# Kernel tuning notes

Measured on AMD Instinct MI355X. Metric: run time of the kernel, lower is better.

The kernel has to match this reference:

```python
import jax, jax.numpy as jnp
import numpy as np

N_NODES = 100000
N_EDGES = 1000000
NODE_DIM = 64
HIDDEN_DIM = 128


def setup_inputs() -> dict:
    key = jax.random.key(0)
    ks = jax.random.split(key, 9)
    x = jax.random.normal(ks[0], (N_NODES, NODE_DIM), dtype=jnp.float32)
    y = jax.random.normal(ks[1], (N_NODES, NODE_DIM), dtype=jnp.float32)
    edge_index = jax.random.randint(ks[2], (2, N_EDGES), 0, N_NODES, dtype=jnp.int64)
    pos_x = jax.random.normal(ks[3], (N_NODES, 3), dtype=jnp.float32)
    pos_y = jax.random.normal(ks[4], (N_NODES, 3), dtype=jnp.float32)
    in_dim = NODE_DIM * 2 + 1
    # Kaiming-uniform-ish init like torch Linear
    lim1 = 1.0 / np.sqrt(in_dim)
    lim2 = 1.0 / np.sqrt(HIDDEN_DIM)
    W1 = jax.random.uniform(ks[5], (in_dim, HIDDEN_DIM), jnp.float32, -lim1, lim1)
    b1 = jax.random.uniform(ks[6], (HIDDEN_DIM,), jnp.float32, -lim1, lim1)
    W2 = jax.random.uniform(ks[7], (HIDDEN_DIM, 1), jnp.float32, -lim2, lim2)
    b2 = jax.random.uniform(ks[8], (1,), jnp.float32, -lim2, lim2)
    return {"x": x, "y": y, "edge_index": edge_index, "pos_x": pos_x,
            "pos_y": pos_y, "W1": W1, "b1": b1, "W2": W2, "b2": b2}


def reference(x, y, edge_index, pos_x, pos_y, W1, b1, W2, b2):
    src = edge_index[0]
    dst = edge_index[1]
    # per-edge euclidean distance between endpoint positions  [E]
    d = pos_x[src] - pos_y[dst]                      # [E, 3]
    dist = jnp.sqrt(jnp.sum(d * d, axis=1))          # [E]
    # gather + concat: [E, node_dim*2 + 1]
    mlp_in = jnp.concatenate([x[src], y[dst], dist[:, None]], axis=1)
    h = jax.nn.relu(mlp_in @ W1 + b1)                # [E, hidden]
    out = jax.nn.relu(h @ W2 + b2)                   # [E, 1]
    return out
```

## Files before the change

### kernel.cpp

```cpp
#include <hip/hip_runtime.h>
#include <hip/hip_bf16.h>


constexpr int NDIM  = 64;
constexpr int HID   = 128;
constexpr int KPAD  = 136;

typedef __attribute__((ext_vector_type(8))) short  short8;
typedef __attribute__((ext_vector_type(4))) int    int4v;
typedef __attribute__((ext_vector_type(4))) float  floatx4;

__device__ __forceinline__ short f2bf(float f) {
    union { __hip_bfloat16 h; short s; } cv;
    cv.h = __float2bfloat16(f);
    return cv.s;
}

__device__ __forceinline__ int pack2(float a, float b) {
    union { __hip_bfloat162 h; int u; } cv;
    cv.h = __float22bfloat162_rn(float2{a, b});
    return cv.u;
}

__global__ __launch_bounds__(256) void edge_mlp_kernel(
    const float* __restrict__ x, const float* __restrict__ y,
    const int*  __restrict__ ei, const float* __restrict__ px,
    const float* __restrict__ py, const float* __restrict__ W1,
    const float* __restrict__ b1, const float* __restrict__ W2,
    const float* __restrict__ b2, float* __restrict__ out, int E)
{
    __shared__ __align__(16) short Wt[HID * KPAD];

    const int tid = threadIdx.x;

    for (int base = 0; base < HID * HID; base += 256 * 8) {
        float f[8];
#pragma unroll
        for (int u = 0; u < 8; ++u) f[u] = W1[base + u * 256 + tid];
#pragma unroll
        for (int u = 0; u < 8; ++u) {
            int i = base + u * 256 + tid;
            Wt[(i & 127) * KPAD + (i >> 7)] = f2bf(f[u]);
        }
    }
    __syncthreads();

    const int lane = tid & 63;
    const int wave = tid >> 6;
    const int quad = lane >> 4;
    const int lm   = lane & 15;

    short8 bfrag[8][4];
#pragma unroll
    for (int t = 0; t < 8; ++t) {
        const int n = t * 16 + lm;
#pragma unroll
        for (int s = 0; s < 4; ++s) {
            const int k0 = s * 32 + quad * 8;
            bfrag[t][s] = *reinterpret_cast<const short8*>(&Wt[n * KPAD + k0]);
        }
    }

    float b1v[8], w2v[8], w1rv[8];
#pragma unroll
    for (int t = 0; t < 8; ++t) {
        const int n = t * 16 + lm;
        b1v[t]  = b1[n];
        w2v[t]  = W2[n];
        w1rv[t] = W1[128 * HID + n];
    }
    const float b2s = b2[0];

    const int* __restrict__ srcp = ei;
    const int* __restrict__ dstp = ei + E;

    const int ntile_cnt = E / 64;
    for (int tile = blockIdx.x; tile < ntile_cnt; tile += gridDim.x) {
        const int m_base = tile * 64 + wave * 16;
        int m = m_base + lm;
        if (m >= E) m = E - 1;
        const int src = srcp[m];
        const int dst = dstp[m];

        const float dx = px[src * 3 + 0] - py[dst * 3 + 0];
        const float dy = px[src * 3 + 1] - py[dst * 3 + 1];
        const float dz = px[src * 3 + 2] - py[dst * 3 + 2];
        const float dist = sqrtf(dx * dx + dy * dy + dz * dz);

        short8 afrag[4];
#pragma unroll
        for (int s = 0; s < 4; ++s) {
            const int kk = s * 32 + quad * 8;
            const float* rp = (s < 2) ? (x + src * NDIM + kk)
                                      : (y + dst * NDIM + (kk - 64));
            const floatx4 f0 = *reinterpret_cast<const floatx4*>(rp);
            const floatx4 f1 = *reinterpret_cast<const floatx4*>(rp + 4);
            union { int4v i; short8 s8; } cv;
            cv.i.x = pack2(f0.x, f0.y);
            cv.i.y = pack2(f0.z, f0.w);
            cv.i.z = pack2(f1.x, f1.y);
            cv.i.w = pack2(f1.z, f1.w);
            afrag[s] = cv.s8;
        }

        floatx4 acc[8];
#pragma unroll
        for (int t = 0; t < 8; ++t) acc[t] = floatx4{0.f, 0.f, 0.f, 0.f};
#pragma unroll
        for (int s = 0; s < 4; ++s) {
#pragma unroll
            for (int t = 0; t < 8; ++t) {
                acc[t] = __builtin_amdgcn_mfma_f32_16x16x32_bf16(
                    afrag[s], bfrag[t][s], acc[t], 0, 0, 0);
            }
        }

        const float dm0 = __shfl(dist, quad * 4 + 0, 64);
        const float dm1 = __shfl(dist, quad * 4 + 1, 64);
        const float dm2 = __shfl(dist, quad * 4 + 2, 64);
        const float dm3 = __shfl(dist, quad * 4 + 3, 64);

        float p0 = 0.f, p1 = 0.f, p2 = 0.f, p3 = 0.f;
#pragma unroll
        for (int t = 0; t < 8; ++t) {
            float h;
            h = acc[t][0] + dm0 * w1rv[t] + b1v[t]; h = fmaxf(h, 0.f); p0 += h * w2v[t];
            h = acc[t][1] + dm1 * w1rv[t] + b1v[t]; h = fmaxf(h, 0.f); p1 += h * w2v[t];
            h = acc[t][2] + dm2 * w1rv[t] + b1v[t]; h = fmaxf(h, 0.f); p2 += h * w2v[t];
            h = acc[t][3] + dm3 * w1rv[t] + b1v[t]; h = fmaxf(h, 0.f); p3 += h * w2v[t];
        }
#pragma unroll
        for (int off = 1; off < 16; off <<= 1) {
            p0 += __shfl_xor(p0, off, 64);
            p1 += __shfl_xor(p1, off, 64);
            p2 += __shfl_xor(p2, off, 64);
            p3 += __shfl_xor(p3, off, 64);
        }
        if (lm < 4) {
            const float v = (lm == 0) ? p0 : (lm == 1) ? p1 : (lm == 2) ? p2 : p3;
            const int e = m_base + quad * 4 + lm;
            if (e < E) out[e] = fmaxf(v + b2s, 0.f);
        }
    }
}

extern "C" void kernel_launch(void* const* d_in, const int* in_sizes, int n_in,
                              void* d_out, int out_size, void* d_ws, size_t ws_size,
                              hipStream_t stream)
{
    const float* x  = (const float*)d_in[0];
    const float* y  = (const float*)d_in[1];
    const int*   ei = (const int*)  d_in[2];
    const float* px = (const float*)d_in[3];
    const float* py = (const float*)d_in[4];
    const float* W1 = (const float*)d_in[5];
    const float* b1 = (const float*)d_in[6];
    const float* W2 = (const float*)d_in[7];
    const float* b2 = (const float*)d_in[8];
    float* out = (float*)d_out;
    const int E = in_sizes[2] / 2;

    edge_mlp_kernel<<<dim3(1024), dim3(256), 0, stream>>>(
        x, y, ei, px, py, W1, b1, W2, b2, out, E);
}
```

Measured before the change: 193.3 us.

## Stream W1 fragments from LDS, fold dist and bias into MFMA, two edge groups per wave

Stops holding all 32 W1 B-fragments in registers. Each B fragment is now read from LDS inside the loop and reused across two 16-edge groups per wave, with tiles growing from 64 to 128 edges. The distance column and bias b1 are folded into a fifth K-slice MFMA (dist, 1.0 padded with zeros), so the per-element FMA epilogue goes away, and the launch moves to 768 blocks with launch_bounds(256,3). The aim is lower register pressure for higher occupancy and more memory-level parallelism on the gathers. In exchange it adds LDS read traffic, an extra MFMA per tile, and bf16 rounding of dist and b1.

```diff
diff --git a/kernel.cpp b/kernel.cpp
--- a/kernel.cpp
+++ b/kernel.cpp
@@ -22,7 +22,18 @@
     return cv.u;
 }
 
-__global__ __launch_bounds__(256) void edge_mlp_kernel(
+__device__ __forceinline__ short8 make_afrag(const float* rp) {
+    const floatx4 f0 = *reinterpret_cast<const floatx4*>(rp);
+    const floatx4 f1 = *reinterpret_cast<const floatx4*>(rp + 4);
+    union { int4v i; short8 s8; } cv;
+    cv.i.x = pack2(f0.x, f0.y);
+    cv.i.y = pack2(f0.z, f0.w);
+    cv.i.z = pack2(f1.x, f1.y);
+    cv.i.w = pack2(f1.z, f1.w);
+    return cv.s8;
+}
+
+__global__ __launch_bounds__(256, 3) void edge_mlp_kernel(
     const float* __restrict__ x, const float* __restrict__ y,
     const int*  __restrict__ ei, const float* __restrict__ px,
     const float* __restrict__ py, const float* __restrict__ W1,
@@ -43,6 +54,13 @@
             Wt[(i & 127) * KPAD + (i >> 7)] = f2bf(f[u]);
         }
     }
+    if (tid < HID) {
+        const int n = tid;
+        Wt[n * KPAD + 128] = f2bf(W1[128 * HID + n]);
+        Wt[n * KPAD + 129] = f2bf(b1[n]);
+#pragma unroll
+        for (int j = 130; j < 136; ++j) Wt[n * KPAD + j] = 0;
+    }
     __syncthreads();
 
     const int lane = tid & 63;
@@ -50,84 +68,94 @@
     const int quad = lane >> 4;
     const int lm   = lane & 15;
 
-    short8 bfrag[8][4];
-#pragma unroll
-    for (int t = 0; t < 8; ++t) {
-        const int n = t * 16 + lm;
-#pragma unroll
-        for (int s = 0; s < 4; ++s) {
-            const int k0 = s * 32 + quad * 8;
-            bfrag[t][s] = *reinterpret_cast<const short8*>(&Wt[n * KPAD + k0]);
-        }
-    }
-
-    float b1v[8], w2v[8], w1rv[8];
-#pragma unroll
-    for (int t = 0; t < 8; ++t) {
-        const int n = t * 16 + lm;
-        b1v[t]  = b1[n];
-        w2v[t]  = W2[n];
-        w1rv[t] = W1[128 * HID + n];
-    }
+    float w2v[8];
+#pragma unroll
+    for (int t = 0; t < 8; ++t) w2v[t] = W2[t * 16 + lm];
     const float b2s = b2[0];
 
     const int* __restrict__ srcp = ei;
     const int* __restrict__ dstp = ei + E;
 
-    const int ntile_cnt = E / 64;
-    for (int tile = blockIdx.x; tile < ntile_cnt; tile += gridDim.x) {
-        const int m_base = tile * 64 + wave * 16;
-        int m = m_base + lm;
-        if (m >= E) m = E - 1;
-        const int src = srcp[m];
-        const int dst = dstp[m];
-
-        const float dx = px[src * 3 + 0] - py[dst * 3 + 0];
-        const float dy = px[src * 3 + 1] - py[dst * 3 + 1];
-        const float dz = px[src * 3 + 2] - py[dst * 3 + 2];
-        const float dist = sqrtf(dx * dx + dy * dy + dz * dz);
-
-        short8 afrag[4];
+    const int sel5 = (quad == 0) ? 128 : 0;
+
+    const int ntiles = (E + 127) / 128;
+    for (int tile = blockIdx.x; tile < ntiles; tile += gridDim.x) {
+        const int mb = tile * 128 + wave * 32;
+        int m0 = mb + lm;       if (m0 >= E) m0 = E - 1;
+        int m1 = mb + 16 + lm;  if (m1 >= E) m1 = E - 1;
+        const int src0 = srcp[m0], dst0 = dstp[m0];
+        const int src1 = srcp[m1], dst1 = dstp[m1];
+
+        const float dx0 = px[src0 * 3 + 0] - py[dst0 * 3 + 0];
+        const float dy0 = px[src0 * 3 + 1] - py[dst0 * 3 + 1];
+        const float dz0 = px[src0 * 3 + 2] - py[dst0 * 3 + 2];
+        const float dist0 = sqrtf(dx0 * dx0 + dy0 * dy0 + dz0 * dz0);
+        const float dx1 = px[src1 * 3 + 0] - py[dst1 * 3 + 0];
+        const float dy1 = px[src1 * 3 + 1] - py[dst1 * 3 + 1];
+        const float dz1 = px[src1 * 3 + 2] - py[dst1 * 3 + 2];
+        const float dist1 = sqrtf(dx1 * dx1 + dy1 * dy1 + dz1 * dz1);
+
+        short8 fa[4], fb[4];
 #pragma unroll
         for (int s = 0; s < 4; ++s) {
             const int kk = s * 32 + quad * 8;
-            const float* rp = (s < 2) ? (x + src * NDIM + kk)
-                                      : (y + dst * NDIM + (kk - 64));
-            const floatx4 f0 = *reinterpret_cast<const floatx4*>(rp);
-            const floatx4 f1 = *reinterpret_cast<const floatx4*>(rp + 4);
-            union { int4v i; short8 s8; } cv;
-            cv.i.x = pack2(f0.x, f0.y);
-            cv.i.y = pack2(f0.z, f0.w);
-            cv.i.z = pack2(f1.x, f1.y);
-            cv.i.w = pack2(f1.z, f1.w);
-            afrag[s] = cv.s8;
-        }
-
-        floatx4 acc[8];
-#pragma unroll
-        for (int t = 0; t < 8; ++t) acc[t] = floatx4{0.f, 0.f, 0.f, 0.f};
-#pragma unroll
-        for (int s = 0; s < 4; ++s) {
-#pragma unroll
-            for (int t = 0; t < 8; ++t) {
-                acc[t] = __builtin_amdgcn_mfma_f32_16x16x32_bf16(
-                    afrag[s], bfrag[t][s], acc[t], 0, 0, 0);
-            }
-        }
-
-        const float dm0 = __shfl(dist, quad * 4 + 0, 64);
-        const float dm1 = __shfl(dist, quad * 4 + 1, 64);
-        const float dm2 = __shfl(dist, quad * 4 + 2, 64);
-        const float dm3 = __shfl(dist, quad * 4 + 3, 64);
+            fa[s] = make_afrag((s < 2) ? (x + src0 * NDIM + kk) : (y + dst0 * NDIM + (kk - 64)));
+            fb[s] = make_afrag((s < 2) ? (x + src1 * NDIM + kk) : (y + dst1 * NDIM + (kk - 64)));
+        }
+        short8 fa4, fb4;
+        {
+            union { int4v i; short8 s8; } ca, cb;
+            const int d0 = (quad == 0) ? pack2(dist0, 1.0f) : 0;
+            const int d1 = (quad == 0) ? pack2(dist1, 1.0f) : 0;
+            ca.i = int4v{d0, 0, 0, 0};
+            cb.i = int4v{d1, 0, 0, 0};
+            fa4 = ca.s8; fb4 = cb.s8;
+        }
+
+        floatx4 accA[8], accB[8];
+#pragma unroll
+        for (int t = 0; t < 8; ++t) {
+            accA[t] = floatx4{0.f, 0.f, 0.f, 0.f};
+            accB[t] = floatx4{0.f, 0.f, 0.f, 0.f};
+        }
+
+        int zoff = 0;
+        asm volatile("" : "+v"(zoff));
+        const short* wr  = Wt + zoff + lm * KPAD + quad * 8;
+        const short* wr5 = Wt + zoff + lm * KPAD + sel5;
+
+#pragma unroll
+        for (int t = 0; t < 8; ++t) {
+            const short* base = wr + t * (16 * KPAD);
+            const short8 bg0 = *reinterpret_cast<const short8*>(base);
+            const short8 bg1 = *reinterpret_cast<const short8*>(base + 32);
+            const short8 bg2 = *reinterpret_cast<const short8*>(base + 64);
+            const short8 bg3 = *reinterpret_cast<const short8*>(base + 96);
+            const short8 bg4 = *reinterpret_cast<const short8*>(wr5 + t * (16 * KPAD));
+            accA[t] = __builtin_amdgcn_mfma_f32_16x16x32_bf16(fa[0], bg0, accA[t], 0, 0, 0);
+            accB[t] = __builtin_amdgcn_mfma_f32_16x16x32_bf16(fb[0], bg0, accB[t], 0, 0, 0);
+            accA[t] = __builtin_amdgcn_mfma_f32_16x16x32_bf16(fa[1], bg1, accA[t], 0, 0, 0);
+            accB[t] = __builtin_amdgcn_mfma_f32_16x16x32_bf16(fb[1], bg1, accB[t], 0, 0, 0);
+            accA[t] = __builtin_amdgcn_mfma_f32_16x16x32_bf16(fa[2], bg2, accA[t], 0, 0, 0);
+            accB[t] = __builtin_amdgcn_mfma_f32_16x16x32_bf16(fb[2], bg2, accB[t], 0, 0, 0);
+            accA[t] = __builtin_amdgcn_mfma_f32_16x16x32_bf16(fa[3], bg3, accA[t], 0, 0, 0);
+            accB[t] = __builtin_amdgcn_mfma_f32_16x16x32_bf16(fb[3], bg3, accB[t], 0, 0, 0);
+            accA[t] = __builtin_amdgcn_mfma_f32_16x16x32_bf16(fa4,  bg4, accA[t], 0, 0, 0);
+            accB[t] = __builtin_amdgcn_mfma_f32_16x16x32_bf16(fb4,  bg4, accB[t], 0, 0, 0);
+        }
 
         float p0 = 0.f, p1 = 0.f, p2 = 0.f, p3 = 0.f;
+        float q0 = 0.f, q1 = 0.f, q2 = 0.f, q3 = 0.f;
 #pragma unroll
         for (int t = 0; t < 8; ++t) {
-            float h;
-            h = acc[t][0] + dm0 * w1rv[t] + b1v[t]; h = fmaxf(h, 0.f); p0 += h * w2v[t];
-            h = acc[t][1] + dm1 * w1rv[t] + b1v[t]; h = fmaxf(h, 0.f); p1 += h * w2v[t];
-            h = acc[t][2] + dm2 * w1rv[t] + b1v[t]; h = fmaxf(h, 0.f); p2 += h * w2v[t];
-            h = acc[t][3] + dm3 * w1rv[t] + b1v[t]; h = fmaxf(h, 0.f); p3 += h * w2v[t];
+            p0 += fmaxf(accA[t][0], 0.f) * w2v[t];
+            p1 += fmaxf(accA[t][1], 0.f) * w2v[t];
+            p2 += fmaxf(accA[t][2], 0.f) * w2v[t];
+            p3 += fmaxf(accA[t][3], 0.f) * w2v[t];
+            q0 += fmaxf(accB[t][0], 0.f) * w2v[t];
+            q1 += fmaxf(accB[t][1], 0.f) * w2v[t];
+            q2 += fmaxf(accB[t][2], 0.f) * w2v[t];
+            q3 += fmaxf(accB[t][3], 0.f) * w2v[t];
         }
 #pragma unroll
         for (int off = 1; off < 16; off <<= 1) {
@@ -135,11 +163,18 @@
             p1 += __shfl_xor(p1, off, 64);
             p2 += __shfl_xor(p2, off, 64);
             p3 += __shfl_xor(p3, off, 64);
+            q0 += __shfl_xor(q0, off, 64);
+            q1 += __shfl_xor(q1, off, 64);
+            q2 += __shfl_xor(q2, off, 64);
+            q3 += __shfl_xor(q3, off, 64);
         }
         if (lm < 4) {
-            const float v = (lm == 0) ? p0 : (lm == 1) ? p1 : (lm == 2) ? p2 : p3;
-            const int e = m_base + quad * 4 + lm;
-            if (e < E) out[e] = fmaxf(v + b2s, 0.f);
+            const float vA = (lm == 0) ? p0 : (lm == 1) ? p1 : (lm == 2) ? p2 : p3;
+            const float vB = (lm == 0) ? q0 : (lm == 1) ? q1 : (lm == 2) ? q2 : q3;
+            const int eA = mb + quad * 4 + lm;
+            const int eB = mb + 16 + quad * 4 + lm;
+            if (eA < E) out[eA] = fmaxf(vA + b2s, 0.f);
+            if (eB < E) out[eB] = fmaxf(vB + b2s, 0.f);
         }
     }
 }
@@ -160,6 +195,6 @@
     float* out = (float*)d_out;
     const int E = in_sizes[2] / 2;
 
-    edge_mlp_kernel<<<dim3(1024), dim3(256), 0, stream>>>(
+    edge_mlp_kernel<<<dim3(768), dim3(256), 0, stream>>>(
         x, y, ei, px, py, W1, b1, W2, b2, out, E);
 }
```

Result: no change. 192.4 us (-0.5%).
